# Performance work log

Hardware: AMD Instinct MI355X
Metric: run time of the kernel (lower is better)

Reference implementation:

```python
import jax, jax.numpy as jnp
import numpy as np

B, N, M = 4, 16384, 4096
C1, C2 = 256, 512
C_IN = C1 + C2  # 768
C_H, C_OUT = 256, 256
EPS_BN = 1e-5
EPS_DIST = 1e-8


def _bn(x, gamma, beta):
    # x: [B, C, n]; training-mode batchnorm (batch statistics over B and n)
    mean = x.mean(axis=(0, 2), keepdims=True)
    var = x.var(axis=(0, 2), keepdims=True)
    return (x - mean) * jax.lax.rsqrt(var + EPS_BN) * gamma[None, :, None] + beta[None, :, None]


def setup_inputs() -> dict:
    key = jax.random.key(0)
    ks = jax.random.split(key, 8)
    inp = {
        "unknown": jax.random.normal(ks[0], (B, N, 3), dtype=jnp.float32),
        "known": jax.random.normal(ks[1], (B, M, 3), dtype=jnp.float32),
        "unknow_feats": jax.random.normal(ks[2], (B, C1, N), dtype=jnp.float32),
        "known_feats": jax.random.normal(ks[3], (B, C2, M), dtype=jnp.float32),
        "W1": jax.random.normal(ks[4], (C_H, C_IN), dtype=jnp.float32) * 0.02,
        "b1": jnp.zeros((C_H,), dtype=jnp.float32),
        "g1": jnp.ones((C_H,), dtype=jnp.float32),
        "bt1": jnp.zeros((C_H,), dtype=jnp.float32),
        "W2": jax.random.normal(ks[5], (C_OUT, C_H), dtype=jnp.float32) * 0.02,
        "b2": jnp.zeros((C_OUT,), dtype=jnp.float32),
        "g2": jnp.ones((C_OUT,), dtype=jnp.float32),
        "bt2": jnp.zeros((C_OUT,), dtype=jnp.float32),
    }
    return inp


def reference(unknown, known, unknow_feats, known_feats,
              W1, b1, g1, bt1, W2, b2, g2, bt2):
    # --- three_nn: brute-force squared distances [B, n, m], take 3 smallest ---
    d2 = jnp.sum((unknown[:, :, None, :] - known[:, None, :, :]) ** 2, axis=-1)
    neg_d, idx = jax.lax.top_k(-d2, 3)          # idx: [B, n, 3]
    dist = -neg_d                                # squared dists (as in CUDA three_nn)
    recip = 1.0 / (dist + EPS_DIST)
    weight = recip / recip.sum(axis=-1, keepdims=True)  # [B, n, 3]
    # --- three_interpolate: weighted gather from known_feats [B, C2, m] ---
    gathered = jax.vmap(lambda f, i: f[:, i])(known_feats, idx)  # [B, C2, n, 3]
    interp = jnp.einsum('bcnk,bnk->bcn', gathered, weight)       # [B, C2, n]
    # --- concat + SharedMLP (1x1 conv -> BN -> ReLU, twice) ---
    x = jnp.concatenate([interp, unknow_feats], axis=1)          # [B, C1+C2, n]
    x = jax.nn.relu(_bn(jnp.einsum('bcn,oc->bon', x, W1) + b1[None, :, None], g1, bt1))
    x = jax.nn.relu(_bn(jnp.einsum('bcn,oc->bon', x, W2) + b2[None, :, None], g2, bt2))
    return x  # [B, mlp[-1], n]
```

## Files before the change

kernel.cpp:

```cpp
#include <hip/hip_runtime.h>
#include <hip/hip_bf16.h>
#include <stdint.h>
#include <stddef.h>

#define B_   4
#define N_   16384
#define M_   4096
#define C1_  256
#define C2_  512
#define CIN_ 768
#define CH_  256
#define NG_  (B_*N_)
#define NSLOT 64

typedef __attribute__((ext_vector_type(8))) short short8;
typedef __attribute__((ext_vector_type(4))) float f32x4;

__device__ __forceinline__ float bf2f(unsigned short u){
  union { unsigned int i; float f; } v; v.i = ((unsigned int)u)<<16; return v.f;
}
__device__ __forceinline__ unsigned short f2bf(float f){
  union { float f; unsigned int i; } v; v.f = f;
  unsigned int r = v.i + 0x7fffu + ((v.i>>16)&1u);
  return (unsigned short)(r>>16);
}

__global__ __launch_bounds__(256) void prep_k(const float* __restrict__ W1,
                                              const float* __restrict__ W2,
                                              const float* __restrict__ kn,
                                              unsigned short* __restrict__ W1b,
                                              unsigned short* __restrict__ W2b,
                                              float4* __restrict__ k4){
  int i = blockIdx.x*256 + threadIdx.x;
  if (i < CIN_*CH_) W1b[i] = f2bf(W1[i]);
  if (i < CH_*CH_)  W2b[i] = f2bf(W2[i]);
  if (i < B_*M_){
    float x = kn[3*i], y = kn[3*i+1], z = kn[3*i+2];
    float4 v; v.x = -2.f*x; v.y = -2.f*y; v.z = -2.f*z; v.w = x*x+y*y+z*z;
    k4[i] = v;
  }
}

__global__ __launch_bounds__(256) void kft_k(const float* __restrict__ kf,
                                             unsigned short* __restrict__ kftb){
  int m0 = blockIdx.x*64, c0 = blockIdx.y*64, b = blockIdx.z;
  __shared__ float tile[64][65];
  int t = threadIdx.x;
  #pragma unroll
  for (int p=0;p<16;p++){
    int row = p*4 + (t>>6), col = t&63;
    tile[row][col] = kf[((size_t)b*C2_ + c0+row)*M_ + m0+col];
  }
  __syncthreads();
  #pragma unroll
  for (int q=0;q<2;q++){
    int id = q*256 + t;
    int ml = id >> 3, c8 = (id & 7)*8;
    short8 o;
    #pragma unroll
    for (int e=0;e<8;++e) o[e] = (short)f2bf(tile[c8+e][ml]);
    *(short8*)(kftb + ((size_t)b*M_ + m0+ml)*C2_ + c0 + c8) = o;
  }
}

__global__ __launch_bounds__(512) void three_nn_k(const float* __restrict__ unk,
                                                  const float4* __restrict__ k4,
                                                  int* __restrict__ idx,
                                                  float* __restrict__ wgt){
  __shared__ __align__(16) char smem[65536];
  float4* kl = (float4*)smem;
  float*  sd = (float*)smem;
  int*    si = (int*)(smem + 24*128*4);
  int b  = blockIdx.x >> 7;
  int n0 = (blockIdx.x & 127) * 128;
  int t = threadIdx.x;
  int w = t >> 6, l = t & 63;
  const float4* src = k4 + (size_t)b*M_;
  #pragma unroll
  for (int i=0;i<8;++i) kl[i*512 + t] = src[i*512 + t];
  const float* upA = unk + ((size_t)b*N_ + n0 + l)*3;
  const float* upB = unk + ((size_t)b*N_ + n0 + 64 + l)*3;
  float ax=upA[0], ay=upA[1], az=upA[2];
  float bx=upB[0], by=upB[1], bz=upB[2];
  __syncthreads();
  float a0=1e30f,a1=1e30f,a2=1e30f; int ia0=0,ia1=0,ia2=0;
  float b0=1e30f,b1=1e30f,b2=1e30f; int ib0=0,ib1=0,ib2=0;
  const float4* kp = kl + w*512;
  const int mbase = w*512;
  #pragma unroll 8
  for (int m=0;m<512;++m){
    float4 kq = kp[m];
    int mi = mbase + m;
    float da = __builtin_fmaf(ax,kq.x, __builtin_fmaf(ay,kq.y, __builtin_fmaf(az,kq.z, kq.w)));
    float db = __builtin_fmaf(bx,kq.x, __builtin_fmaf(by,kq.y, __builtin_fmaf(bz,kq.z, kq.w)));
    {
      bool c0 = da < a0, c1 = da < a1, c2 = da < a2;
      int tA = c1 ? ia1 : mi;  ia2 = c2 ? tA : ia2;
      int tB = c0 ? ia0 : mi;  ia1 = c1 ? tB : ia1;
      ia0 = c0 ? mi : ia0;
      float n1 = __builtin_amdgcn_fmed3f(da, a0, a1);
      float n2 = __builtin_amdgcn_fmed3f(da, a1, a2);
      a0 = fminf(da, a0); a1 = n1; a2 = n2;
    }
    {
      bool c0 = db < b0, c1 = db < b1, c2 = db < b2;
      int tA = c1 ? ib1 : mi;  ib2 = c2 ? tA : ib2;
      int tB = c0 ? ib0 : mi;  ib1 = c1 ? tB : ib1;
      ib0 = c0 ? mi : ib0;
      float n1 = __builtin_amdgcn_fmed3f(db, b0, b1);
      float n2 = __builtin_amdgcn_fmed3f(db, b1, b2);
      b0 = fminf(db, b0); b1 = n1; b2 = n2;
    }
  }
  __syncthreads();
  sd[(w*3+0)*128 + l] = a0;  sd[(w*3+0)*128 + 64 + l] = b0;
  sd[(w*3+1)*128 + l] = a1;  sd[(w*3+1)*128 + 64 + l] = b1;
  sd[(w*3+2)*128 + l] = a2;  sd[(w*3+2)*128 + 64 + l] = b2;
  si[(w*3+0)*128 + l] = ia0; si[(w*3+0)*128 + 64 + l] = ib0;
  si[(w*3+1)*128 + l] = ia1; si[(w*3+1)*128 + 64 + l] = ib1;
  si[(w*3+2)*128 + l] = ia2; si[(w*3+2)*128 + 64 + l] = ib2;
  __syncthreads();
  if (t < 128) {
    float bd0=1e30f,bd1=1e30f,bd2=1e30f; int bi0=0,bi1=0,bi2=0;
    #pragma unroll
    for (int q=0;q<24;++q){
      float d = sd[q*128 + t]; int ii = si[q*128 + t];
      bool c0 = d < bd0, c1 = d < bd1, c2 = d < bd2;
      int tA = c1 ? bi1 : ii;  bi2 = c2 ? tA : bi2;
      int tB = c0 ? bi0 : ii;  bi1 = c1 ? tB : bi1;
      bi0 = c0 ? ii : bi0;
      float nd1 = __builtin_amdgcn_fmed3f(d, bd0, bd1);
      float nd2 = __builtin_amdgcn_fmed3f(d, bd1, bd2);
      bd0 = fminf(d, bd0); bd1 = nd1; bd2 = nd2;
    }
    int np = n0 + t;
    const float* upt = unk + ((size_t)b*N_ + np)*3;
    float x = upt[0], y = upt[1], z = upt[2];
    float uu0 = x*x + y*y + z*z;
    float t0 = fmaxf(bd0 + uu0, 0.f) + 1e-8f;
    float t1 = fmaxf(bd1 + uu0, 0.f) + 1e-8f;
    float t2 = fmaxf(bd2 + uu0, 0.f) + 1e-8f;
    float r0 = 1.f/t0, r1 = 1.f/t1, r2 = 1.f/t2;
    float s = r0+r1+r2;
    size_t gp = ((size_t)b*N_ + np)*3;
    idx[gp]=bi0; idx[gp+1]=bi1; idx[gp+2]=bi2;
    wgt[gp]=r0/s; wgt[gp+1]=r1/s; wgt[gp+2]=r2/s;
  }
}

__global__ __launch_bounds__(256) void uft_k(const float* __restrict__ uf,
                                             unsigned short* __restrict__ uft){
  int b  = blockIdx.x >> 8;
  int n0 = (blockIdx.x & 255) * 64;
  int t = threadIdx.x;
  __shared__ float tile[64][65];
  for (int cc=0; cc<4; ++cc){
    int c0 = cc*64;
    __syncthreads();
    #pragma unroll
    for (int p=0;p<16;p++){
      int row = p*4 + (t>>6), col = t&63;
      tile[row][col] = uf[((size_t)b*C1_ + c0+row)*N_ + n0+col];
    }
    __syncthreads();
    #pragma unroll
    for (int q=0;q<2;q++){
      int id = q*256 + t;
      int nl = id >> 3, c8 = (id & 7)*8;
      short8 o;
      #pragma unroll
      for (int e=0;e<8;++e) o[e] = (short)f2bf(tile[c8+e][nl]);
      *(short8*)(uft + ((size_t)b*N_ + n0+nl)*CH_ + c0 + c8) = o;
    }
  }
}

template<int KTOT, int MODE>
__global__ __launch_bounds__(256) void gemm_bt_k(const unsigned short* __restrict__ Wb,
                                                 const unsigned short* __restrict__ Bt,
                                                 unsigned short* __restrict__ Yt,
                                                 float* __restrict__ sump,
                                                 float* __restrict__ sqp,
                                                 const float* __restrict__ scalep,
                                                 const float* __restrict__ shiftp,
                                                 const unsigned short* __restrict__ kftb,
                                                 const int* __restrict__ idx,
                                                 const float* __restrict__ wgt){
  __shared__ short lsA[128*64];
  __shared__ short lsB[128*64];
  const int t = threadIdx.x, w = t>>6, l = t&63;
  const int nBase = (blockIdx.x>>1)*128, oBase = (blockIdx.x&1)*128;
  const int wm = w>>1, wn = w&1, rl = l&15, hi = l>>4;
  f32x4 acc[4][4];
  #pragma unroll
  for (int i=0;i<4;i++)
    #pragma unroll
    for (int j=0;j<4;j++) acc[i][j] = (f32x4){0.f,0.f,0.f,0.f};
  const int srow8 = l>>3, sch = l&7;
  int jj0[4], jj1[4], jj2[4];
  float ww0[4], ww1[4], ww2[4];
  const unsigned short* kfb = nullptr;
  if constexpr (MODE == 1){
    kfb = kftb + (size_t)(nBase >> 14)*M_*C2_;
    #pragma unroll
    for (int j=0;j<4;++j){
      int row = w*8 + j*32 + srow8;
      size_t gp = (size_t)(nBase + row)*3;
      jj0[j] = idx[gp];   jj1[j] = idx[gp+1];   jj2[j] = idx[gp+2];
      ww0[j] = wgt[gp];   ww1[j] = wgt[gp+1];   ww2[j] = wgt[gp+2];
    }
  }
  for (int ks=0; ks<KTOT/64; ++ks){
    const int k0 = ks*64;
    __syncthreads();
    #pragma unroll
    for (int j=0;j<4;++j){
      int row = w*8 + j*32 + srow8;
      const unsigned short* gA = Wb + (size_t)(oBase+row)*KTOT + k0 + ((sch ^ (row&7))<<3);
      __builtin_amdgcn_global_load_lds((const __attribute__((address_space(1))) unsigned int*)gA,
          (__attribute__((address_space(3))) unsigned int*)(lsA + w*512 + j*2048), 16, 0, 0);
      if constexpr (MODE == 1){
        if (k0 >= C2_){
          const unsigned short* gB = Bt + (size_t)(nBase+row)*CH_ + (k0 - C2_) + ((sch ^ (row&7))<<3);
          __builtin_amdgcn_global_load_lds((const __attribute__((address_space(1))) unsigned int*)gB,
              (__attribute__((address_space(3))) unsigned int*)(lsB + w*512 + j*2048), 16, 0, 0);
        }
      }
    }
    if constexpr (MODE == 1){
      if (k0 < C2_){
        #pragma unroll
        for (int j=0;j<4;++j){
          int row = w*8 + j*32 + srow8;
          int chb = k0 + ((sch ^ (row&7))<<3);
          const short8 a0 = *(const short8*)(kfb + (size_t)jj0[j]*C2_ + chb);
          const short8 a1 = *(const short8*)(kfb + (size_t)jj1[j]*C2_ + chb);
          const short8 a2 = *(const short8*)(kfb + (size_t)jj2[j]*C2_ + chb);
          float w0 = ww0[j], w1 = ww1[j], w2 = ww2[j];
          short8 o;
          #pragma unroll
          for (int e=0;e<8;++e){
            float f = w0*bf2f((unsigned short)a0[e])
                    + w1*bf2f((unsigned short)a1[e])
                    + w2*bf2f((unsigned short)a2[e]);
            o[e] = (short)f2bf(f);
          }
          *(short8*)(lsB + w*512 + j*2048 + l*8) = o;
        }
      }
    }
    if constexpr (MODE == 2){
      #pragma unroll
      for (int j=0;j<4;++j){
        int row = w*8 + j*32 + srow8;
        int chb = k0 + ((sch ^ (row&7))<<3);
        const short8 v = *(const short8*)(Bt + (size_t)(nBase+row)*KTOT + chb);
        float4 sc0 = *(const float4*)(scalep + chb);
        float4 sc1 = *(const float4*)(scalep + chb + 4);
        float4 sh0 = *(const float4*)(shiftp + chb);
        float4 sh1 = *(const float4*)(shiftp + chb + 4);
        short8 o;
        float f0 = bf2f((unsigned short)v[0])*sc0.x + sh0.x; o[0] = (short)f2bf(f0 > 0.f ? f0 : 0.f);
        float f1 = bf2f((unsigned short)v[1])*sc0.y + sh0.y; o[1] = (short)f2bf(f1 > 0.f ? f1 : 0.f);
        float f2 = bf2f((unsigned short)v[2])*sc0.z + sh0.z; o[2] = (short)f2bf(f2 > 0.f ? f2 : 0.f);
        float f3 = bf2f((unsigned short)v[3])*sc0.w + sh0.w; o[3] = (short)f2bf(f3 > 0.f ? f3 : 0.f);
        float f4 = bf2f((unsigned short)v[4])*sc1.x + sh1.x; o[4] = (short)f2bf(f4 > 0.f ? f4 : 0.f);
        float f5 = bf2f((unsigned short)v[5])*sc1.y + sh1.y; o[5] = (short)f2bf(f5 > 0.f ? f5 : 0.f);
        float f6 = bf2f((unsigned short)v[6])*sc1.z + sh1.z; o[6] = (short)f2bf(f6 > 0.f ? f6 : 0.f);
        float f7 = bf2f((unsigned short)v[7])*sc1.w + sh1.w; o[7] = (short)f2bf(f7 > 0.f ? f7 : 0.f);
        *(short8*)(lsB + w*512 + j*2048 + l*8) = o;
      }
    }
    __syncthreads();
    #pragma unroll
    for (int kk=0;kk<2;++kk){
      short8 af[4], bfr[4];
      const int pc = ((kk*4 + hi) ^ (rl&7)) << 3;
      #pragma unroll
      for (int mi=0;mi<4;++mi) af[mi]  = *(const short8*)(lsA + (wm*64 + mi*16 + rl)*64 + pc);
      #pragma unroll
      for (int ni=0;ni<4;++ni) bfr[ni] = *(const short8*)(lsB + (wn*64 + ni*16 + rl)*64 + pc);
      #pragma unroll
      for (int mi=0;mi<4;++mi)
        #pragma unroll
        for (int ni=0;ni<4;++ni)
          acc[mi][ni] = __builtin_amdgcn_mfma_f32_16x16x32_bf16(af[mi], bfr[ni], acc[mi][ni], 0,0,0);
    }
  }
  #pragma unroll
  for (int mi=0;mi<4;++mi)
    #pragma unroll
    for (int ni=0;ni<4;++ni){
      int n = nBase + wn*64 + ni*16 + rl;
      int o = oBase + wm*64 + mi*16 + hi*4;
      unsigned int lo = (unsigned int)f2bf(acc[mi][ni][0]) | ((unsigned int)f2bf(acc[mi][ni][1])<<16);
      unsigned int hi2= (unsigned int)f2bf(acc[mi][ni][2]) | ((unsigned int)f2bf(acc[mi][ni][3])<<16);
      uint2 vv; vv.x = lo; vv.y = hi2;
      *(uint2*)(Yt + (size_t)n*256 + o) = vv;
    }
  float s_[4][4], q_[4][4];
  #pragma unroll
  for (int mi=0;mi<4;++mi)
    #pragma unroll
    for (int j=0;j<4;++j){
      float s0 = acc[mi][0][j] + acc[mi][1][j] + acc[mi][2][j] + acc[mi][3][j];
      float q0 = acc[mi][0][j]*acc[mi][0][j];
      q0 = __builtin_fmaf(acc[mi][1][j], acc[mi][1][j], q0);
      q0 = __builtin_fmaf(acc[mi][2][j], acc[mi][2][j], q0);
      q0 = __builtin_fmaf(acc[mi][3][j], acc[mi][3][j], q0);
      s_[mi][j] = s0; q_[mi][j] = q0;
    }
  #pragma unroll
  for (int off=1; off<16; off<<=1){
    #pragma unroll
    for (int mi=0;mi<4;++mi)
      #pragma unroll
      for (int j=0;j<4;++j){
        s_[mi][j] += __shfl_xor(s_[mi][j], off);
        q_[mi][j] += __shfl_xor(q_[mi][j], off);
      }
  }
  if (rl == 0){
    const int slot = (blockIdx.x>>1) & (NSLOT-1);
    #pragma unroll
    for (int mi=0;mi<4;++mi)
      #pragma unroll
      for (int j=0;j<4;++j){
        int o = oBase + wm*64 + mi*16 + hi*4 + j;
        atomicAdd(&sump[slot*256 + o], s_[mi][j]);
        atomicAdd(&sqp[slot*256 + o],  q_[mi][j]);
      }
  }
}

__global__ __launch_bounds__(256) void finalize_k(const float* __restrict__ sump,
                                                  const float* __restrict__ sqp,
                                                  const float* __restrict__ g,
                                                  const float* __restrict__ bt,
                                                  float* __restrict__ scale,
                                                  float* __restrict__ shift){
  int t = threadIdx.x;
  float s = 0.f, q = 0.f;
  #pragma unroll 8
  for (int k=0;k<NSLOT;++k){
    s += sump[k*256 + t];
    q += sqp[k*256 + t];
  }
  float mean = s * (1.f/65536.f);
  float var  = q * (1.f/65536.f) - mean*mean;
  float sc = g[t] * rsqrtf(var + 1e-5f);
  scale[t] = sc;
  shift[t] = bt[t] - mean*sc;
}

__global__ __launch_bounds__(256) void out_k(const unsigned short* __restrict__ Yt,
                                             const float* __restrict__ scale,
                                             const float* __restrict__ shift,
                                             float* __restrict__ out){
  int gn0 = blockIdx.x*64;
  int o0  = blockIdx.y*64;
  int b = gn0 >> 14, n0 = gn0 & (N_-1);
  __shared__ unsigned short tile[64][66];
  int t = threadIdx.x;
  #pragma unroll
  for (int p=0;p<4;++p){
    int nl = p*16 + (t>>4), ol = (t&15)*4;
    const unsigned short* src = Yt + (size_t)(gn0+nl)*256 + o0 + ol;
    uint2 vv = *(const uint2*)src;
    tile[nl][ol+0] = (unsigned short)(vv.x & 0xffff);
    tile[nl][ol+1] = (unsigned short)(vv.x >> 16);
    tile[nl][ol+2] = (unsigned short)(vv.y & 0xffff);
    tile[nl][ol+3] = (unsigned short)(vv.y >> 16);
  }
  __syncthreads();
  #pragma unroll
  for (int p=0;p<4;++p){
    int ol = p*16 + (t>>4), nl = (t&15)*4;
    float sc = scale[o0+ol], sh = shift[o0+ol];
    float4 r;
    float f0 = bf2f(tile[nl+0][ol])*sc + sh; r.x = f0 > 0.f ? f0 : 0.f;
    float f1 = bf2f(tile[nl+1][ol])*sc + sh; r.y = f1 > 0.f ? f1 : 0.f;
    float f2v= bf2f(tile[nl+2][ol])*sc + sh; r.z = f2v > 0.f ? f2v : 0.f;
    float f3 = bf2f(tile[nl+3][ol])*sc + sh; r.w = f3 > 0.f ? f3 : 0.f;
    *(float4*)(out + ((size_t)(b*256 + o0+ol))*N_ + n0 + nl) = r;
  }
}

extern "C" void kernel_launch(void* const* d_in, const int* in_sizes, int n_in,
                              void* d_out, int out_size, void* d_ws, size_t ws_size,
                              hipStream_t stream) {
  const float* unknown     = (const float*)d_in[0];
  const float* known       = (const float*)d_in[1];
  const float* unknow_f    = (const float*)d_in[2];
  const float* known_f     = (const float*)d_in[3];
  const float* W1          = (const float*)d_in[4];
  const float* g1          = (const float*)d_in[6];
  const float* bt1         = (const float*)d_in[7];
  const float* W2          = (const float*)d_in[8];
  const float* g2          = (const float*)d_in[10];
  const float* bt2         = (const float*)d_in[11];
  float* out = (float*)d_out;

  char* ws = (char*)d_ws;
  const size_t szUft  = (size_t)NG_*CH_*2;
  const size_t szY    = (size_t)NG_*256*2;
  const size_t szKftb = (size_t)B_*M_*C2_*2;
  const size_t szIdx  = (size_t)NG_*3*4;
  const size_t szPart = (size_t)NSLOT*256*4;
  const size_t o_Uft  = 0;
  const size_t o_Y    = szUft;
  const size_t o_kftb = o_Y + szY;
  const size_t o_idx  = o_kftb + szKftb;
  const size_t o_wgt  = o_idx + szIdx;
  const size_t o_W1b  = o_wgt + szIdx;
  const size_t o_W2b  = o_W1b + (size_t)CIN_*CH_*2;
  const size_t o_st   = o_W2b + (size_t)CH_*CH_*2;
  const size_t o_k4   = o_st + 4*szPart + 4*256*sizeof(float);

  unsigned short* Uft  = (unsigned short*)(ws + o_Uft);
  unsigned short* Y2   = (unsigned short*)(ws + o_Uft);
  unsigned short* Y    = (unsigned short*)(ws + o_Y);
  unsigned short* kftb = (unsigned short*)(ws + o_kftb);
  int*            idx  = (int*)(ws + o_idx);
  float*          wgt  = (float*)(ws + o_wgt);
  unsigned short* W1b  = (unsigned short*)(ws + o_W1b);
  unsigned short* W2b  = (unsigned short*)(ws + o_W2b);
  float* st = (float*)(ws + o_st);
  float4* k4 = (float4*)(ws + o_k4);
  float *sum1p = st;
  float *sq1p  = st + NSLOT*256;
  float *sum2p = st + 2*NSLOT*256;
  float *sq2p  = st + 3*NSLOT*256;
  float *scale1 = st + 4*NSLOT*256;
  float *shift1 = scale1 + 256;
  float *scale2 = scale1 + 512;
  float *shift2 = scale1 + 768;

  hipMemsetAsync(st, 0, 4*szPart, stream);

  prep_k<<<768, 256, 0, stream>>>(W1, W2, known, W1b, W2b, k4);
  kft_k<<<dim3(M_/64, C2_/64, B_), 256, 0, stream>>>(known_f, kftb);
  three_nn_k<<<B_*(N_/128), 512, 0, stream>>>(unknown, k4, idx, wgt);
  uft_k<<<B_*(N_/64), 256, 0, stream>>>(unknow_f, Uft);

  gemm_bt_k<CIN_, 1><<<NG_/64, 256, 0, stream>>>(W1b, Uft, Y, sum1p, sq1p,
                                                 nullptr, nullptr, kftb, idx, wgt);
  finalize_k<<<1, 256, 0, stream>>>(sum1p, sq1p, g1, bt1, scale1, shift1);

  gemm_bt_k<CH_, 2><<<NG_/64, 256, 0, stream>>>(W2b, Y, Y2, sum2p, sq2p,
                                                scale1, shift1, nullptr, nullptr, nullptr);
  finalize_k<<<1, 256, 0, stream>>>(sum2p, sq2p, g2, bt2, scale2, shift2);
  out_k<<<dim3(NG_/64, 4), 256, 0, stream>>>(Y2, scale2, shift2, out);
}
```

Baseline: 259.3 us.

## Fuse unknown-feature transpose into first GEMM and use intrinsic bf16 conversion

Removes the separate transpose/convert kernel for unknow_feats and instead has the first GEMM load fp32 features directly from the [C1,N] layout, converting to bf16 while staging into LDS. This eliminates an intermediate bf16 buffer write and reread plus a kernel launch. The GEMM's B-operand loads become strided register loads instead of async global-to-LDS copies, which may reduce load efficiency. The manual round-to-nearest bf16 conversion is replaced with the HIP intrinsic.

```diff
diff --git a/kernel.cpp b/kernel.cpp
--- a/kernel.cpp
+++ b/kernel.cpp
@@ -19,10 +19,9 @@
 __device__ __forceinline__ float bf2f(unsigned short u){
   union { unsigned int i; float f; } v; v.i = ((unsigned int)u)<<16; return v.f;
 }
-__device__ __forceinline__ unsigned short f2bf(float f){
-  union { float f; unsigned int i; } v; v.f = f;
-  unsigned int r = v.i + 0x7fffu + ((v.i>>16)&1u);
-  return (unsigned short)(r>>16);
+__device__ __forceinline__ unsigned short f2bfh(float f){
+  __hip_bfloat16 h = __float2bfloat16(f);
+  return *reinterpret_cast<unsigned short*>(&h);
 }
 
 __global__ __launch_bounds__(256) void prep_k(const float* __restrict__ W1,
@@ -32,8 +31,8 @@
                                               unsigned short* __restrict__ W2b,
                                               float4* __restrict__ k4){
   int i = blockIdx.x*256 + threadIdx.x;
-  if (i < CIN_*CH_) W1b[i] = f2bf(W1[i]);
-  if (i < CH_*CH_)  W2b[i] = f2bf(W2[i]);
+  if (i < CIN_*CH_) W1b[i] = f2bfh(W1[i]);
+  if (i < CH_*CH_)  W2b[i] = f2bfh(W2[i]);
   if (i < B_*M_){
     float x = kn[3*i], y = kn[3*i+1], z = kn[3*i+2];
     float4 v; v.x = -2.f*x; v.y = -2.f*y; v.z = -2.f*z; v.w = x*x+y*y+z*z;
@@ -58,7 +57,7 @@
     int ml = id >> 3, c8 = (id & 7)*8;
     short8 o;
     #pragma unroll
-    for (int e=0;e<8;++e) o[e] = (short)f2bf(tile[c8+e][ml]);
+    for (int e=0;e<8;++e) o[e] = (short)f2bfh(tile[c8+e][ml]);
     *(short8*)(kftb + ((size_t)b*M_ + m0+ml)*C2_ + c0 + c8) = o;
   }
 }
@@ -148,33 +147,6 @@
   }
 }
 
-__global__ __launch_bounds__(256) void uft_k(const float* __restrict__ uf,
-                                             unsigned short* __restrict__ uft){
-  int b  = blockIdx.x >> 8;
-  int n0 = (blockIdx.x & 255) * 64;
-  int t = threadIdx.x;
-  __shared__ float tile[64][65];
-  for (int cc=0; cc<4; ++cc){
-    int c0 = cc*64;
-    __syncthreads();
-    #pragma unroll
-    for (int p=0;p<16;p++){
-      int row = p*4 + (t>>6), col = t&63;
-      tile[row][col] = uf[((size_t)b*C1_ + c0+row)*N_ + n0+col];
-    }
-    __syncthreads();
-    #pragma unroll
-    for (int q=0;q<2;q++){
-      int id = q*256 + t;
-      int nl = id >> 3, c8 = (id & 7)*8;
-      short8 o;
-      #pragma unroll
-      for (int e=0;e<8;++e) o[e] = (short)f2bf(tile[c8+e][nl]);
-      *(short8*)(uft + ((size_t)b*N_ + n0+nl)*CH_ + c0 + c8) = o;
-    }
-  }
-}
-
 template<int KTOT, int MODE>
 __global__ __launch_bounds__(256) void gemm_bt_k(const unsigned short* __restrict__ Wb,
                                                  const unsigned short* __restrict__ Bt,
@@ -185,7 +157,8 @@
                                                  const float* __restrict__ shiftp,
                                                  const unsigned short* __restrict__ kftb,
                                                  const int* __restrict__ idx,
-                                                 const float* __restrict__ wgt){
+                                                 const float* __restrict__ wgt,
+                                                 const float* __restrict__ uff){
   __shared__ short lsA[128*64];
   __shared__ short lsB[128*64];
   const int t = threadIdx.x, w = t>>6, l = t&63;
@@ -200,8 +173,13 @@
   int jj0[4], jj1[4], jj2[4];
   float ww0[4], ww1[4], ww2[4];
   const unsigned short* kfb = nullptr;
+  const float* ufb = nullptr;
+  int nloc = 0;
   if constexpr (MODE == 1){
-    kfb = kftb + (size_t)(nBase >> 14)*M_*C2_;
+    int bb = nBase >> 14;
+    nloc = nBase & (N_-1);
+    kfb = kftb + (size_t)bb*M_*C2_;
+    ufb = uff + (size_t)bb*C1_*N_;
     #pragma unroll
     for (int j=0;j<4;++j){
       int row = w*8 + j*32 + srow8;
@@ -219,13 +197,6 @@
       const unsigned short* gA = Wb + (size_t)(oBase+row)*KTOT + k0 + ((sch ^ (row&7))<<3);
       __builtin_amdgcn_global_load_lds((const __attribute__((address_space(1))) unsigned int*)gA,
           (__attribute__((address_space(3))) unsigned int*)(lsA + w*512 + j*2048), 16, 0, 0);
-      if constexpr (MODE == 1){
-        if (k0 >= C2_){
-          const unsigned short* gB = Bt + (size_t)(nBase+row)*CH_ + (k0 - C2_) + ((sch ^ (row&7))<<3);
-          __builtin_amdgcn_global_load_lds((const __attribute__((address_space(1))) unsigned int*)gB,
-              (__attribute__((address_space(3))) unsigned int*)(lsB + w*512 + j*2048), 16, 0, 0);
-        }
-      }
     }
     if constexpr (MODE == 1){
       if (k0 < C2_){
@@ -243,8 +214,19 @@
             float f = w0*bf2f((unsigned short)a0[e])
                     + w1*bf2f((unsigned short)a1[e])
                     + w2*bf2f((unsigned short)a2[e]);
-            o[e] = (short)f2bf(f);
+            o[e] = (short)f2bfh(f);
           }
+          *(short8*)(lsB + w*512 + j*2048 + l*8) = o;
+        }
+      } else {
+        #pragma unroll
+        for (int j=0;j<4;++j){
+          int row = w*8 + j*32 + srow8;
+          int cb = (k0 - C2_) + ((sch ^ (row&7))<<3);
+          const float* up = ufb + (size_t)cb*N_ + (nloc + row);
+          short8 o;
+          #pragma unroll
+          for (int e=0;e<8;++e) o[e] = (short)f2bfh(up[(size_t)e*N_]);
           *(short8*)(lsB + w*512 + j*2048 + l*8) = o;
         }
       }
@@ -260,14 +242,14 @@
         float4 sh0 = *(const float4*)(shiftp + chb);
         float4 sh1 = *(const float4*)(shiftp + chb + 4);
         short8 o;
-        float f0 = bf2f((unsigned short)v[0])*sc0.x + sh0.x; o[0] = (short)f2bf(f0 > 0.f ? f0 : 0.f);
-        float f1 = bf2f((unsigned short)v[1])*sc0.y + sh0.y; o[1] = (short)f2bf(f1 > 0.f ? f1 : 0.f);
-        float f2 = bf2f((unsigned short)v[2])*sc0.z + sh0.z; o[2] = (short)f2bf(f2 > 0.f ? f2 : 0.f);
-        float f3 = bf2f((unsigned short)v[3])*sc0.w + sh0.w; o[3] = (short)f2bf(f3 > 0.f ? f3 : 0.f);
-        float f4 = bf2f((unsigned short)v[4])*sc1.x + sh1.x; o[4] = (short)f2bf(f4 > 0.f ? f4 : 0.f);
-        float f5 = bf2f((unsigned short)v[5])*sc1.y + sh1.y; o[5] = (short)f2bf(f5 > 0.f ? f5 : 0.f);
-        float f6 = bf2f((unsigned short)v[6])*sc1.z + sh1.z; o[6] = (short)f2bf(f6 > 0.f ? f6 : 0.f);
-        float f7 = bf2f((unsigned short)v[7])*sc1.w + sh1.w; o[7] = (short)f2bf(f7 > 0.f ? f7 : 0.f);
+        float f0 = bf2f((unsigned short)v[0])*sc0.x + sh0.x; o[0] = (short)f2bfh(f0 > 0.f ? f0 : 0.f);
+        float f1 = bf2f((unsigned short)v[1])*sc0.y + sh0.y; o[1] = (short)f2bfh(f1 > 0.f ? f1 : 0.f);
+        float f2 = bf2f((unsigned short)v[2])*sc0.z + sh0.z; o[2] = (short)f2bfh(f2 > 0.f ? f2 : 0.f);
+        float f3 = bf2f((unsigned short)v[3])*sc0.w + sh0.w; o[3] = (short)f2bfh(f3 > 0.f ? f3 : 0.f);
+        float f4 = bf2f((unsigned short)v[4])*sc1.x + sh1.x; o[4] = (short)f2bfh(f4 > 0.f ? f4 : 0.f);
+        float f5 = bf2f((unsigned short)v[5])*sc1.y + sh1.y; o[5] = (short)f2bfh(f5 > 0.f ? f5 : 0.f);
+        float f6 = bf2f((unsigned short)v[6])*sc1.z + sh1.z; o[6] = (short)f2bfh(f6 > 0.f ? f6 : 0.f);
+        float f7 = bf2f((unsigned short)v[7])*sc1.w + sh1.w; o[7] = (short)f2bfh(f7 > 0.f ? f7 : 0.f);
         *(short8*)(lsB + w*512 + j*2048 + l*8) = o;
       }
     }
@@ -293,8 +275,8 @@
     for (int ni=0;ni<4;++ni){
       int n = nBase + wn*64 + ni*16 + rl;
       int o = oBase + wm*64 + mi*16 + hi*4;
-      unsigned int lo = (unsigned int)f2bf(acc[mi][ni][0]) | ((unsigned int)f2bf(acc[mi][ni][1])<<16);
-      unsigned int hi2= (unsigned int)f2bf(acc[mi][ni][2]) | ((unsigned int)f2bf(acc[mi][ni][3])<<16);
+      unsigned int lo = (unsigned int)f2bfh(acc[mi][ni][0]) | ((unsigned int)f2bfh(acc[mi][ni][1])<<16);
+      unsigned int hi2= (unsigned int)f2bfh(acc[mi][ni][2]) | ((unsigned int)f2bfh(acc[mi][ni][3])<<16);
       uint2 vv; vv.x = lo; vv.y = hi2;
       *(uint2*)(Yt + (size_t)n*256 + o) = vv;
     }
@@ -402,13 +384,12 @@
   float* out = (float*)d_out;
 
   char* ws = (char*)d_ws;
-  const size_t szUft  = (size_t)NG_*CH_*2;
   const size_t szY    = (size_t)NG_*256*2;
   const size_t szKftb = (size_t)B_*M_*C2_*2;
   const size_t szIdx  = (size_t)NG_*3*4;
   const size_t szPart = (size_t)NSLOT*256*4;
-  const size_t o_Uft  = 0;
-  const size_t o_Y    = szUft;
+  const size_t o_Y2   = 0;
+  const size_t o_Y    = szY;
   const size_t o_kftb = o_Y + szY;
   const size_t o_idx  = o_kftb + szKftb;
   const size_t o_wgt  = o_idx + szIdx;
@@ -417,8 +398,7 @@
   const size_t o_st   = o_W2b + (size_t)CH_*CH_*2;
   const size_t o_k4   = o_st + 4*szPart + 4*256*sizeof(float);
 
-  unsigned short* Uft  = (unsigned short*)(ws + o_Uft);
-  unsigned short* Y2   = (unsigned short*)(ws + o_Uft);
+  unsigned short* Y2   = (unsigned short*)(ws + o_Y2);
   unsigned short* Y    = (unsigned short*)(ws + o_Y);
   unsigned short* kftb = (unsigned short*)(ws + o_kftb);
   int*            idx  = (int*)(ws + o_idx);
@@ -441,14 +421,13 @@
   prep_k<<<768, 256, 0, stream>>>(W1, W2, known, W1b, W2b, k4);
   kft_k<<<dim3(M_/64, C2_/64, B_), 256, 0, stream>>>(known_f, kftb);
   three_nn_k<<<B_*(N_/128), 512, 0, stream>>>(unknown, k4, idx, wgt);
-  uft_k<<<B_*(N_/64), 256, 0, stream>>>(unknow_f, Uft);
-
-  gemm_bt_k<CIN_, 1><<<NG_/64, 256, 0, stream>>>(W1b, Uft, Y, sum1p, sq1p,
-                                                 nullptr, nullptr, kftb, idx, wgt);
+
+  gemm_bt_k<CIN_, 1><<<NG_/64, 256, 0, stream>>>(W1b, nullptr, Y, sum1p, sq1p,
+                                                 nullptr, nullptr, kftb, idx, wgt, unknow_f);
   finalize_k<<<1, 256, 0, stream>>>(sum1p, sq1p, g1, bt1, scale1, shift1);
 
   gemm_bt_k<CH_, 2><<<NG_/64, 256, 0, stream>>>(W2b, Y, Y2, sum2p, sq2p,
-                                                scale1, shift1, nullptr, nullptr, nullptr);
+                                                scale1, shift1, nullptr, nullptr, nullptr, nullptr);
   finalize_k<<<1, 256, 0, stream>>>(sum2p, sq2p, g2, bt2, scale2, shift2);
   out_k<<<dim3(NG_/64, 4), 256, 0, stream>>>(Y2, scale2, shift2, out);
 }
```

New measurement: 288.0 us. 11.1% more time.
